# Kernel tuning notes

Hardware: AMD Instinct MI355X
Metric: run time of the kernel (lower is better)

Reference implementation:

```python
import jax, jax.numpy as jnp
import numpy as np

B, S, D, H, HD = 2, 2048, 2048, 16, 128

def _freqs_cis(dim, end, theta=10000.0):
    freqs = 1.0 / theta ** (np.arange(0, dim, 2, dtype=np.float32)[: dim // 2] / dim)
    t = np.arange(end, dtype=np.float32)
    f = np.outer(t, freqs).astype(np.float32)
    f = np.concatenate((f, f), axis=-1)
    return jnp.asarray(np.cos(f)), jnp.asarray(np.sin(f))

def _rotate_half(x):
    x1, x2 = x[..., : x.shape[-1] // 2], x[..., x.shape[-1] // 2 :]
    return jnp.concatenate((-x2, x1), axis=-1)

def setup_inputs() -> dict:
    key = jax.random.key(0)
    ks = jax.random.split(key, 5)
    x = jax.random.normal(ks[0], (B, S, D), jnp.float32)
    scale = 1.0 / np.sqrt(D)
    Wq = jax.random.normal(ks[1], (D, H, HD), jnp.float32) * scale
    Wk = jax.random.normal(ks[2], (D, H, HD), jnp.float32) * scale
    Wv = jax.random.normal(ks[3], (D, H, HD), jnp.float32) * scale
    Wo = jax.random.normal(ks[4], (H, HD, D), jnp.float32) * (1.0 / np.sqrt(D))
    mask = jnp.tril(jnp.ones((S, S), jnp.bool_))[None, None]  # causal [1,1,S,S]
    return {"x": x, "mask": mask, "Wq": Wq, "Wk": Wk, "Wv": Wv, "Wo": Wo}

def reference(x, mask, Wq, Wk, Wv, Wo):
    # QKV projections: [B,S,D] -> [B,S,H,HD]
    q = jnp.einsum('bsd,dhk->bshk', x, Wq)
    k = jnp.einsum('bsd,dhk->bshk', x, Wk)
    v = jnp.einsum('bsd,dhk->bshk', x, Wv)
    # RoPE
    cos, sin = _freqs_cis(HD, x.shape[1])
    cos = cos[None, :, None, :]
    sin = sin[None, :, None, :]
    q = q * cos + _rotate_half(q) * sin
    k = k * cos + _rotate_half(k) * sin
    # scaled dot-product attention
    scores = jnp.einsum('bqhk,bshk->bhqs', q, k) / jnp.sqrt(jnp.asarray(HD, q.dtype))
    big_neg = jnp.finfo(scores.dtype).min
    scores = jnp.where(mask, scores, big_neg)
    attn = jax.nn.softmax(scores, axis=-1)
    ctx = jnp.einsum('bhqs,bshk->bqhk', attn, v)
    # output projection contracting (heads, head_dim)
    return jnp.einsum('bqhk,hkd->bqd', ctx, Wo)
```

## Files before the change

### kernel.cpp

```cpp
#include <hip/hip_runtime.h>

typedef unsigned short u16;
typedef unsigned int u32;

constexpr int Bc = 2, Sc = 2048, Dc = 2048, Hc = 16, HDc = 128;

using short8 = __attribute__((ext_vector_type(8))) short;
using f32x4v = __attribute__((ext_vector_type(4))) float;

static __device__ __forceinline__ float bf2f(u16 v) { return __uint_as_float(((u32)v) << 16); }
static __device__ __forceinline__ u16 f2bf(float f) {
    u32 u = __float_as_uint(f);
    return (u16)((u + 0x7fffu + ((u >> 16) & 1u)) >> 16);
}

__device__ __forceinline__ void gll16(const u16* g, u16* l) {
    __builtin_amdgcn_global_load_lds((const __attribute__((address_space(1))) void*)g,
                                     (__attribute__((address_space(3))) void*)l, 16, 0, 0);
}

__global__ __launch_bounds__(256) void rope_tab_k(float* __restrict__ ctab, float* __restrict__ stab) {
    int idx = blockIdx.x * 256 + threadIdx.x;
    int s = idx >> 6, i = idx & 63;
    float freq = exp2f(-(float)i * 0.20762050593045952f);
    float ang = (float)s * freq;
    float c, sn;
    sincosf(ang, &sn, &c);
    ctab[idx] = c;
    stab[idx] = sn;
}

__global__ __launch_bounds__(256) void cvt_k(const float* __restrict__ in, u16* __restrict__ out, int n) {
    int i = (blockIdx.x * 256 + threadIdx.x) * 8;
    if (i >= n) return;
    float4 a = *(const float4*)(in + i);
    float4 b = *(const float4*)(in + i + 4);
    u16 r[8] = {f2bf(a.x), f2bf(a.y), f2bf(a.z), f2bf(a.w),
                f2bf(b.x), f2bf(b.y), f2bf(b.z), f2bf(b.w)};
    *(uint4*)(out + i) = *(uint4*)r;
}

__global__ __launch_bounds__(256) void tcvt3_k(const float* __restrict__ in0, const float* __restrict__ in1,
                                               const float* __restrict__ in2, u16* __restrict__ out,
                                               int R, int C) {
    __shared__ u16 tile[64][68];
    const float* in = (blockIdx.z == 0) ? in0 : (blockIdx.z == 1) ? in1 : in2;
    u16* o = out + (size_t)blockIdx.z * R * C;
    int bx = blockIdx.x * 64, by = blockIdx.y * 64;
    int t = threadIdx.x;
    int r = t >> 4, c4 = (t & 15) * 4;
    #pragma unroll
    for (int i = 0; i < 4; ++i) {
        int row = by + r + i * 16;
        float4 v = *(const float4*)(in + (size_t)row * C + bx + c4);
        u16* d = &tile[r + i * 16][c4];
        d[0] = f2bf(v.x); d[1] = f2bf(v.y); d[2] = f2bf(v.z); d[3] = f2bf(v.w);
    }
    __syncthreads();
    int oc = t >> 4, r4 = (t & 15) * 4;
    #pragma unroll
    for (int i = 0; i < 4; ++i) {
        int orow = oc + i * 16;
        u16 v[4] = {tile[r4][orow], tile[r4 + 1][orow], tile[r4 + 2][orow], tile[r4 + 3][orow]};
        *(uint2*)&o[(size_t)(bx + orow) * R + by + r4] = *(const uint2*)v;
    }
}

template <int MODE>
__global__ __launch_bounds__(256) void gemm_bt(const u16* __restrict__ A, const u16* __restrict__ Bt,
                                               float* __restrict__ C2, u16* __restrict__ Oq,
                                               u16* __restrict__ Ok, u16* __restrict__ Ov,
                                               const float* __restrict__ ctab,
                                               const float* __restrict__ stab,
                                               int M, int N, int K) {
    __shared__ u16 SM[(MODE == 1) ? 16640 : 8192];
    u16* As = SM;
    u16* Bs = SM + 4096;
    int m0 = blockIdx.y * 128, n0 = blockIdx.x * 128;
    int t = threadIdx.x;
    int wid = t >> 6, lane = t & 63;
    int wr = wid >> 1, wc = wid & 1;
    f32x4v acc[4][4] = {};

    int c0 = wid * 128 + lane;
    int c1 = wid * 128 + 64 + lane;
    const u16* Ar0 = A + (size_t)(m0 + (c0 >> 2)) * K + (((c0 & 3) ^ ((c0 >> 3) & 3)) * 8);
    const u16* Ar1 = A + (size_t)(m0 + (c1 >> 2)) * K + (((c1 & 3) ^ ((c1 >> 3) & 3)) * 8);
    const u16* Br0 = Bt + (size_t)(n0 + (c0 >> 2)) * K + (((c0 & 3) ^ ((c0 >> 3) & 3)) * 8);
    const u16* Br1 = Bt + (size_t)(n0 + (c1 >> 2)) * K + (((c1 & 3) ^ ((c1 >> 3) & 3)) * 8);
    u16* Al0 = As + (size_t)(wid * 128) * 8;
    u16* Al1 = As + (size_t)(wid * 128 + 64) * 8;
    u16* Bl0 = Bs + (size_t)(wid * 128) * 8;
    u16* Bl1 = Bs + (size_t)(wid * 128 + 64) * 8;

    int sw = (lane >> 1) & 3;
    const u16* ap = As + (wr * 64 + (lane & 15)) * 32 + ((((lane >> 4)) ^ sw) << 3);
    const u16* bp = Bs + (wc * 64 + (lane & 15)) * 32 + ((((lane >> 4)) ^ sw) << 3);

    for (int kk = 0; kk < K; kk += 32) {
        gll16(Ar0 + kk, Al0);
        gll16(Ar1 + kk, Al1);
        gll16(Br0 + kk, Bl0);
        gll16(Br1 + kk, Bl1);
        __syncthreads();
        short8 a[4], b[4];
        #pragma unroll
        for (int i = 0; i < 4; ++i) {
            a[i] = *(const short8*)(ap + i * 512);
            b[i] = *(const short8*)(bp + i * 512);
        }
        #pragma unroll
        for (int mf = 0; mf < 4; ++mf)
            #pragma unroll
            for (int nf = 0; nf < 4; ++nf)
                acc[mf][nf] = __builtin_amdgcn_mfma_f32_16x16x32_bf16(a[mf], b[nf], acc[mf][nf], 0, 0, 0);
        __syncthreads();
    }

    int ln = lane & 15, lq = lane >> 4;
    if (MODE == 2) {
        int rb = m0 + wr * 64 + (lq << 2);
        int cb = n0 + wc * 64 + ln;
        #pragma unroll
        for (int mf = 0; mf < 4; ++mf)
            #pragma unroll
            for (int nf = 0; nf < 4; ++nf)
                #pragma unroll
                for (int r = 0; r < 4; ++r)
                    C2[(size_t)(rb + mf * 16 + r) * N + cb + nf * 16] = acc[mf][nf][r];
        return;
    }

    u16* Es = SM;
    {
        int rl0 = wr * 64 + (lq << 2), cl0 = wc * 64 + ln;
        #pragma unroll
        for (int mf = 0; mf < 4; ++mf)
            #pragma unroll
            for (int nf = 0; nf < 4; ++nf)
                #pragma unroll
                for (int r = 0; r < 4; ++r)
                    Es[(rl0 + mf * 16 + r) * 130 + cl0 + nf * 16] = f2bf(acc[mf][nf][r]);
    }
    __syncthreads();

    int which = n0 >> 11;
    int h = (n0 & 2047) >> 7;
    int b_ = m0 >> 11;
    int s0 = m0 & (Sc - 1);

    if (which < 2) {
        u16* dst0 = which ? Ok : Oq;
        int r = t >> 1, h2 = t & 1;
        int s = s0 + r;
        const u16* row = Es + r * 130;
        const float* ct = ctab + (size_t)s * 64;
        const float* st = stab + (size_t)s * 64;
        u16* dp = dst0 + (((size_t)(b_ * Hc + h)) * Sc + s) * HDc + h2 * 64;
        #pragma unroll
        for (int j8 = 0; j8 < 64; j8 += 8) {
            uint4 aa = *(const uint4*)(row + j8);
            uint4 bb = *(const uint4*)(row + 64 + j8);
            const u16* ap8 = (const u16*)&aa;
            const u16* bp8 = (const u16*)&bb;
            float4 c0 = *(const float4*)(ct + j8);
            float4 c1 = *(const float4*)(ct + j8 + 4);
            float4 sn0 = *(const float4*)(st + j8);
            float4 sn1 = *(const float4*)(st + j8 + 4);
            const float* cf = (const float*)&c0;
            float cc[8] = {c0.x, c0.y, c0.z, c0.w, c1.x, c1.y, c1.z, c1.w};
            float ss[8] = {sn0.x, sn0.y, sn0.z, sn0.w, sn1.x, sn1.y, sn1.z, sn1.w};
            (void)cf;
            u16 ov[8];
            #pragma unroll
            for (int e = 0; e < 8; ++e) {
                float x1 = bf2f(ap8[e]), x2 = bf2f(bp8[e]);
                ov[e] = h2 ? f2bf(x2 * cc[e] + x1 * ss[e]) : f2bf(x1 * cc[e] - x2 * ss[e]);
            }
            *(uint4*)(dp + j8) = *(const uint4*)ov;
        }
    } else {
        int d = t >> 1, sh = t & 1;
        u16* dp = Ov + (((size_t)(b_ * Hc + h)) * HDc + d) * Sc + s0 + sh * 64;
        #pragma unroll
        for (int r8 = 0; r8 < 64; r8 += 8) {
            u16 ov[8];
            #pragma unroll
            for (int e = 0; e < 8; ++e)
                ov[e] = Es[(sh * 64 + r8 + e) * 130 + d];
            *(uint4*)(dp + r8) = *(const uint4*)ov;
        }
    }
}

__global__ __launch_bounds__(256) void fattn_k(const u16* __restrict__ Q, const u16* __restrict__ K,
                                               const u16* __restrict__ Vt, u16* __restrict__ ctx) {
    __shared__ u16 KsA[8192];
    __shared__ u16 VsA[8192];
    __shared__ u16 PsA[4 * 32 * 72];
    int t = threadIdx.x, wid = t >> 6, lane = t & 63;
    int bh = blockIdx.x;
    int yt = blockIdx.y;
    int qi = (yt < 8) ? yt : 23 - yt;
    int q0 = qi << 7;
    int wrow0 = q0 + wid * 32;
    const u16* Qb = Q + ((size_t)bh * Sc + wrow0) * HDc;
    const u16* Kb = K + (size_t)bh * Sc * HDc;
    const u16* Vb = Vt + (size_t)bh * HDc * Sc;
    int ln = lane & 15, lq = lane >> 4;
    u16* psw = PsA + wid * 32 * 72;

    short8 aq[2][4];
    #pragma unroll
    for (int mf = 0; mf < 2; ++mf)
        #pragma unroll
        for (int ks = 0; ks < 4; ++ks)
            aq[mf][ks] = *(const short8*)(Qb + (size_t)(mf * 16 + ln) * HDc + ks * 32 + lq * 8);

    short8 onesb;
    {
        short v = (ln == 0) ? (short)0x3F80 : (short)0;
        #pragma unroll
        for (int e = 0; e < 8; ++e) onesb[e] = v;
    }

    f32x4v o[2][8] = {};
    f32x4v lacc[2] = {};

    const float sc = 0.08838834764831845f;
    const float SHIFT = 12.0f;
    int jendw = wrow0 + 31;
    int jendb = q0 + 127;
    int swz = (ln >> 1) & 3;

    for (int j0 = 0; j0 <= jendb; j0 += 64) {
        #pragma unroll
        for (int i = 0; i < 4; ++i) {
            int p = (wid * 4 + i) * 64 + lane;
            int plane = p >> 8, key = (p >> 2) & 63;
            int qc = (p & 3) ^ ((key >> 1) & 3);
            gll16(Kb + (size_t)(j0 + key) * HDc + plane * 32 + qc * 8,
                  KsA + (size_t)(wid * 4 + i) * 512);
        }
        #pragma unroll
        for (int i = 0; i < 4; ++i) {
            int p = (wid * 4 + i) * 64 + lane;
            int plane = p >> 9, d = (p >> 2) & 127;
            int qc = (p & 3) ^ ((d >> 1) & 3);
            gll16(Vb + (size_t)d * Sc + j0 + plane * 32 + qc * 8,
                  VsA + (size_t)(wid * 4 + i) * 512);
        }
        __syncthreads();

        if (j0 <= jendw) {
            f32x4v sf[2][4] = {};
            #pragma unroll
            for (int ks = 0; ks < 4; ++ks)
                #pragma unroll
                for (int nf = 0; nf < 4; ++nf) {
                    short8 bk = *(const short8*)(KsA + ks * 2048 + (nf * 16 + ln) * 32 + ((lq ^ swz) << 3));
                    sf[0][nf] = __builtin_amdgcn_mfma_f32_16x16x32_bf16(aq[0][ks], bk, sf[0][nf], 0, 0, 0);
                    sf[1][nf] = __builtin_amdgcn_mfma_f32_16x16x32_bf16(aq[1][ks], bk, sf[1][nf], 0, 0, 0);
                }

            bool diag = (j0 + 63 > wrow0);
            #pragma unroll
            for (int mf = 0; mf < 2; ++mf) {
                int rowb = mf * 16 + (lq << 2);
                #pragma unroll
                for (int nf = 0; nf < 4; ++nf) {
                    int col = nf * 16 + ln;
                    int ck = col >> 3, cl = col & 7;
                    #pragma unroll
                    for (int r = 0; r < 4; ++r) {
                        float p = __expf(fmaf(sf[mf][nf][r], sc, -SHIFT));
                        if (diag && (j0 + col > wrow0 + rowb + r)) p = 0.f;
                        int row = rowb + r;
                        psw[row * 72 + ((ck ^ (row & 7)) << 3) + cl] = f2bf(p);
                    }
                }
            }

            short8 ap0[2][2];
            #pragma unroll
            for (int mf = 0; mf < 2; ++mf)
                #pragma unroll
                for (int ks = 0; ks < 2; ++ks)
                    ap0[mf][ks] = *(const short8*)(psw + (mf * 16 + ln) * 72 + (((ks * 4 + lq) ^ (ln & 7)) << 3));
            #pragma unroll
            for (int ks = 0; ks < 2; ++ks) {
                lacc[0] = __builtin_amdgcn_mfma_f32_16x16x32_bf16(ap0[0][ks], onesb, lacc[0], 0, 0, 0);
                lacc[1] = __builtin_amdgcn_mfma_f32_16x16x32_bf16(ap0[1][ks], onesb, lacc[1], 0, 0, 0);
                #pragma unroll
                for (int nd = 0; nd < 8; ++nd) {
                    short8 bv = *(const short8*)(VsA + ks * 4096 + (nd * 16 + ln) * 32 + ((lq ^ swz) << 3));
                    o[0][nd] = __builtin_amdgcn_mfma_f32_16x16x32_bf16(ap0[0][ks], bv, o[0][nd], 0, 0, 0);
                    o[1][nd] = __builtin_amdgcn_mfma_f32_16x16x32_bf16(ap0[1][ks], bv, o[1][nd], 0, 0, 0);
                }
            }
        }
        __syncthreads();
    }

    int b = bh >> 4, h = bh & 15;
    #pragma unroll
    for (int mf = 0; mf < 2; ++mf)
        #pragma unroll
        for (int r = 0; r < 4; ++r) {
            float lv = __shfl(lacc[mf][r], lane & 48, 64);
            float inv = 1.0f / lv;
            int q = wrow0 + mf * 16 + (lq << 2) + r;
            u16* cp = ctx + (((size_t)(b * Sc + q)) * Hc + h) * HDc + ln;
            #pragma unroll
            for (int nd = 0; nd < 8; ++nd)
                cp[nd * 16] = f2bf(o[mf][nd][r] * inv);
        }
}

extern "C" void kernel_launch(void* const* d_in, const int* in_sizes, int n_in,
                              void* d_out, int out_size, void* d_ws, size_t ws_size,
                              hipStream_t stream) {
    (void)in_sizes; (void)n_in; (void)out_size; (void)ws_size;
    const float* x  = (const float*)d_in[0];
    const float* Wq = (const float*)d_in[2];
    const float* Wk = (const float*)d_in[3];
    const float* Wv = (const float*)d_in[4];
    const float* Wo = (const float*)d_in[5];

    char* w = (char*)d_ws;
    u16* Wt  = (u16*)w; w += (size_t)3 * Dc * Dc * 2;
    u16* Qb  = (u16*)w; w += (size_t)Bc * Hc * Sc * HDc * 2;
    u16* Kb  = (u16*)w; w += (size_t)Bc * Hc * Sc * HDc * 2;
    u16* Vb  = (u16*)w; w += (size_t)Bc * Hc * Sc * HDc * 2;
    u16* ctx = (u16*)w; w += (size_t)Bc * Sc * Hc * HDc * 2;
    float* ctab = (float*)w; w += (size_t)Sc * 64 * 4;
    float* stab = (float*)w; w += (size_t)Sc * 64 * 4;
    u16* xb = (u16*)d_out;

    rope_tab_k<<<dim3(Sc * 64 / 256), 256, 0, stream>>>(ctab, stab);

    int nx = Bc * Sc * Dc;
    cvt_k<<<dim3(nx / 2048), 256, 0, stream>>>(x, xb, nx);

    tcvt3_k<<<dim3(Dc / 64, Dc / 64, 3), 256, 0, stream>>>(Wq, Wk, Wv, Wt, Dc, Dc);
    gemm_bt<1><<<dim3(3 * Dc / 128, (Bc * Sc) / 128), 256, 0, stream>>>(
        xb, Wt, nullptr, Qb, Kb, Vb, ctab, stab, Bc * Sc, 3 * Dc, Dc);

    fattn_k<<<dim3(Bc * Hc, Sc / 128), 256, 0, stream>>>(Qb, Kb, Vb, ctx);

    tcvt3_k<<<dim3(Dc / 64, Dc / 64, 1), 256, 0, stream>>>(Wo, Wo, Wo, Wt, Dc, Dc);
    gemm_bt<2><<<dim3(Dc / 128, (Bc * Sc) / 128), 256, 0, stream>>>(
        ctx, Wt, (float*)d_out, nullptr, nullptr, nullptr, nullptr, nullptr, Bc * Sc, Dc, Dc);
}
```

Measured before the change: 440.5 us.

## Add 256x256 tiled QKV GEMM with pipelined LDS staging and fused RoPE

Replaces the 128x128 QKV projection GEMM with a new 512-thread kernel that computes 256x256 output tiles. It double-buffers K-slices in LDS through direct global-to-LDS loads, uses an XOR swizzle, and interleaves MFMA quarters with barriers and setprio so memory and compute overlap. The epilogue still applies RoPE and the V transpose, now in two halves through shared memory. The aim is more data reuse per block and better latency hiding, at the cost of higher register and LDS use, fewer blocks in the grid, and hand-tuned waitcnt counts that are fragile.

```diff
diff --git a/kernel.cpp b/kernel.cpp
--- a/kernel.cpp
+++ b/kernel.cpp
@@ -163,14 +163,12 @@
             uint4 bb = *(const uint4*)(row + 64 + j8);
             const u16* ap8 = (const u16*)&aa;
             const u16* bp8 = (const u16*)&bb;
-            float4 c0 = *(const float4*)(ct + j8);
-            float4 c1 = *(const float4*)(ct + j8 + 4);
+            float4 c0f = *(const float4*)(ct + j8);
+            float4 c1f = *(const float4*)(ct + j8 + 4);
             float4 sn0 = *(const float4*)(st + j8);
             float4 sn1 = *(const float4*)(st + j8 + 4);
-            const float* cf = (const float*)&c0;
-            float cc[8] = {c0.x, c0.y, c0.z, c0.w, c1.x, c1.y, c1.z, c1.w};
+            float cc[8] = {c0f.x, c0f.y, c0f.z, c0f.w, c1f.x, c1f.y, c1f.z, c1f.w};
             float ss[8] = {sn0.x, sn0.y, sn0.z, sn0.w, sn1.x, sn1.y, sn1.z, sn1.w};
-            (void)cf;
             u16 ov[8];
             #pragma unroll
             for (int e = 0; e < 8; ++e) {
@@ -190,6 +188,179 @@
                 ov[e] = Es[(sh * 64 + r8 + e) * 130 + d];
             *(uint4*)(dp + r8) = *(const uint4*)ov;
         }
+    }
+}
+
+
+#define FENCE asm volatile("" ::: "memory")
+
+#define RDA(P, mh) do { _Pragma("unroll") for (int m_ = 0; m_ < 4; ++m_) { \
+    aF[m_][0] = *(const short8*)((P) + (mh) * 4096 + m_ * 1024 + co0); \
+    aF[m_][1] = *(const short8*)((P) + (mh) * 4096 + m_ * 1024 + co1); } } while (0)
+
+#define RDB(P, nh) do { _Pragma("unroll") for (int n_ = 0; n_ < 2; ++n_) { \
+    bF[(nh) * 2 + n_][0] = *(const short8*)((P) + ((nh) * 2 + n_) * 1024 + co0); \
+    bF[(nh) * 2 + n_][1] = *(const short8*)((P) + ((nh) * 2 + n_) * 1024 + co1); } } while (0)
+
+#define MFQ(mh, nh) do { _Pragma("unroll") for (int m_ = 0; m_ < 4; ++m_) { \
+    _Pragma("unroll") for (int n_ = 0; n_ < 2; ++n_) { \
+    f32x4v& c_ = acc[(mh) * 4 + m_][(nh) * 2 + n_]; \
+    c_ = __builtin_amdgcn_mfma_f32_16x16x32_bf16(aF[m_][0], bF[(nh) * 2 + n_][0], c_, 0, 0, 0); \
+    c_ = __builtin_amdgcn_mfma_f32_16x16x32_bf16(aF[m_][1], bF[(nh) * 2 + n_][1], c_, 0, 0, 0); } } } while (0)
+
+#define PTAIL(mh, nh) do { FENCE; __builtin_amdgcn_s_barrier(); FENCE; \
+    asm volatile("s_waitcnt lgkmcnt(0)" ::: "memory"); \
+    __builtin_amdgcn_s_setprio(1); MFQ(mh, nh); __builtin_amdgcn_s_setprio(0); \
+    FENCE; __builtin_amdgcn_s_barrier(); FENCE; } while (0)
+
+__global__ __launch_bounds__(512, 2) void gemm256_qkv(
+        const u16* __restrict__ A, const u16* __restrict__ Bt,
+        u16* __restrict__ Oq, u16* __restrict__ Ok, u16* __restrict__ Ov,
+        const float* __restrict__ ctab, const float* __restrict__ stab) {
+    __shared__ u16 SM[65536];
+    constexpr int K = Dc;
+    int t = threadIdx.x, wid = t >> 6, lane = t & 63;
+    int wm = wid >> 2, wn = wid & 3;
+    int ln = lane & 15, lq = lane >> 4;
+
+    int nx = gridDim.x;
+    int lin = blockIdx.y * nx + blockIdx.x;
+    int cpx = (nx * gridDim.y) >> 3;
+    int swzb = (lin & 7) * cpx + (lin >> 3);
+    int n0 = (swzb % nx) << 8;
+    int m0 = (swzb / nx) << 8;
+
+    u16* As0 = SM;
+    u16* As1 = SM + 16384;
+    u16* Bs0 = SM + 32768;
+    u16* Bs1 = SM + 49152;
+
+    auto stage = [&](const u16* G, int r0, int kt, u16* tile, int H) {
+        #pragma unroll
+        for (int L = 0; L < 2; ++L) {
+            int ch16 = H * 1024 + L * 512 + wid * 64 + lane;
+            int row = ch16 >> 3, ch = ch16 & 7;
+            const u16* g = G + (size_t)(r0 + row) * K + kt * 64 + ((ch ^ (row & 7)) << 3);
+            gll16(g, tile + (H * 1024 + L * 512 + wid * 64) * 8);
+        }
+    };
+
+    stage(Bt, n0, 0, Bs0, 0);
+    stage(Bt, n0, 0, Bs0, 1);
+    stage(A,  m0, 0, As0, 0);
+    stage(A,  m0, 0, As0, 1);
+    stage(Bt, n0, 1, Bs1, 0);
+    stage(A,  m0, 1, As1, 0);
+
+    const u16* aR0 = SM + (wm * 128 + ln) * 64;
+    const u16* aR1 = aR0 + 16384;
+    const u16* bR0 = SM + 32768 + (wn * 64 + ln) * 64;
+    const u16* bR1 = bR0 + 16384;
+    int sw = ln & 7;
+    int co0 = (lq ^ sw) << 3;
+    int co1 = ((4 | lq) ^ sw) << 3;
+
+    short8 aF[4][2], bF[4][2];
+    f32x4v acc[8][4] = {};
+
+    asm volatile("s_waitcnt vmcnt(4)" ::: "memory");
+    FENCE; __builtin_amdgcn_s_barrier(); FENCE;
+
+    for (int it = 0; it < K / 128; ++it) {
+        int k1 = (2 * it + 1) & 31, k2 = (2 * it + 2) & 31, k3 = (2 * it + 3) & 31;
+        RDA(aR0, 0); RDB(bR0, 0);
+        stage(Bt, n0, k1, Bs1, 1);
+        asm volatile("s_waitcnt lgkmcnt(8)" ::: "memory");
+        PTAIL(0, 0);
+        RDB(bR0, 1);
+        stage(A, m0, k1, As1, 1);
+        PTAIL(0, 1);
+        RDA(aR0, 1);
+        stage(Bt, n0, k2, Bs0, 0);
+        PTAIL(1, 0);
+        stage(A, m0, k2, As0, 0);
+        asm volatile("s_waitcnt vmcnt(4)" ::: "memory");
+        PTAIL(1, 1);
+        RDA(aR1, 0); RDB(bR1, 0);
+        stage(Bt, n0, k2, Bs0, 1);
+        asm volatile("s_waitcnt lgkmcnt(8)" ::: "memory");
+        PTAIL(0, 0);
+        RDB(bR1, 1);
+        stage(A, m0, k2, As0, 1);
+        PTAIL(0, 1);
+        RDA(aR1, 1);
+        stage(Bt, n0, k3, Bs1, 0);
+        PTAIL(1, 0);
+        stage(A, m0, k3, As1, 0);
+        asm volatile("s_waitcnt vmcnt(4)" ::: "memory");
+        PTAIL(1, 1);
+    }
+    asm volatile("s_waitcnt vmcnt(0)" ::: "memory");
+    __syncthreads();
+
+    int which = n0 >> 11;
+    int h0 = (n0 & 2047) >> 7;
+    int b_ = m0 >> 11;
+    int s0 = m0 & (Sc - 1);
+    u16* Es = SM;
+    const int ESTR = 258;
+
+    #pragma unroll
+    for (int Hh = 0; Hh < 2; ++Hh) {
+        if (wm == Hh) {
+            #pragma unroll
+            for (int mf = 0; mf < 8; ++mf)
+                #pragma unroll
+                for (int nf = 0; nf < 4; ++nf)
+                    #pragma unroll
+                    for (int r = 0; r < 4; ++r)
+                        Es[(mf * 16 + (lq << 2) + r) * ESTR + wn * 64 + nf * 16 + ln] =
+                            f2bf(acc[mf][nf][r]);
+        }
+        __syncthreads();
+        if (which < 2) {
+            u16* dst0 = which ? Ok : Oq;
+            int u = t >> 1, h2 = t & 1;
+            int r = u & 127, hh = u >> 7;
+            int s = s0 + Hh * 128 + r;
+            const u16* rowp = Es + r * ESTR + hh * 128;
+            const float* ct = ctab + (size_t)s * 64;
+            const float* st = stab + (size_t)s * 64;
+            u16* dp = dst0 + (((size_t)(b_ * Hc + h0 + hh)) * Sc + s) * HDc + h2 * 64;
+            #pragma unroll
+            for (int j8 = 0; j8 < 64; j8 += 8) {
+                uint4 aa = *(const uint4*)(rowp + j8);
+                uint4 bb = *(const uint4*)(rowp + 64 + j8);
+                const u16* ap8 = (const u16*)&aa;
+                const u16* bp8 = (const u16*)&bb;
+                float4 c0f = *(const float4*)(ct + j8);
+                float4 c1f = *(const float4*)(ct + j8 + 4);
+                float4 sn0 = *(const float4*)(st + j8);
+                float4 sn1 = *(const float4*)(st + j8 + 4);
+                float cc[8] = {c0f.x, c0f.y, c0f.z, c0f.w, c1f.x, c1f.y, c1f.z, c1f.w};
+                float ss[8] = {sn0.x, sn0.y, sn0.z, sn0.w, sn1.x, sn1.y, sn1.z, sn1.w};
+                u16 ov[8];
+                #pragma unroll
+                for (int e = 0; e < 8; ++e) {
+                    float x1 = bf2f(ap8[e]), x2 = bf2f(bp8[e]);
+                    ov[e] = h2 ? f2bf(x2 * cc[e] + x1 * ss[e]) : f2bf(x1 * cc[e] - x2 * ss[e]);
+                }
+                *(uint4*)(dp + j8) = *(const uint4*)ov;
+            }
+        } else {
+            int u = t >> 1, sh = t & 1;
+            int d = u & 127, hh = u >> 7;
+            u16* dp = Ov + (((size_t)(b_ * Hc + h0 + hh)) * HDc + d) * Sc + s0 + Hh * 128 + sh * 64;
+            #pragma unroll
+            for (int r8 = 0; r8 < 64; r8 += 8) {
+                u16 ov[8];
+                #pragma unroll
+                for (int e = 0; e < 8; ++e)
+                    ov[e] = Es[(sh * 64 + r8 + e) * ESTR + hh * 128 + d];
+                *(uint4*)(dp + r8) = *(const uint4*)ov;
+            }
+        }
+        __syncthreads();
     }
 }
 
@@ -343,8 +514,8 @@
     cvt_k<<<dim3(nx / 2048), 256, 0, stream>>>(x, xb, nx);
 
     tcvt3_k<<<dim3(Dc / 64, Dc / 64, 3), 256, 0, stream>>>(Wq, Wk, Wv, Wt, Dc, Dc);
-    gemm_bt<1><<<dim3(3 * Dc / 128, (Bc * Sc) / 128), 256, 0, stream>>>(
-        xb, Wt, nullptr, Qb, Kb, Vb, ctab, stab, Bc * Sc, 3 * Dc, Dc);
+    gemm256_qkv<<<dim3(3 * Dc / 256, (Bc * Sc) / 256), 512, 0, stream>>>(
+        xb, Wt, Qb, Kb, Vb, ctab, stab);
 
     fattn_k<<<dim3(Bc * Hc, Sc / 128), 256, 0, stream>>>(Qb, Kb, Vb, ctx);
 
```

Result: faster. 424.3 us (-3.7%).

## Replace QKV GEMM with triple-buffered 128x256 tile kernel and XCD-aware block swizzle

Applied to the files above, without the earlier changes.

Adds a dedicated QKV projection GEMM using 512 threads per block and 128x256 output tiles. It stages K in 64-wide slices through a three-stage LDS ring with explicit vmcnt waits, barriers and MFMA priority hints, so loads overlap compute. It also remaps block indices across 8 groups for cache locality. The RoPE/transpose epilogue now handles two heads per block. The cost is much larger LDS use (~144KB) and lower occupancy, which hurts if latency hiding falls short.

```diff
diff --git a/kernel.cpp b/kernel.cpp
--- a/kernel.cpp
+++ b/kernel.cpp
@@ -68,12 +68,9 @@
 
 template <int MODE>
 __global__ __launch_bounds__(256) void gemm_bt(const u16* __restrict__ A, const u16* __restrict__ Bt,
-                                               float* __restrict__ C2, u16* __restrict__ Oq,
-                                               u16* __restrict__ Ok, u16* __restrict__ Ov,
-                                               const float* __restrict__ ctab,
-                                               const float* __restrict__ stab,
+                                               float* __restrict__ C2,
                                                int M, int N, int K) {
-    __shared__ u16 SM[(MODE == 1) ? 16640 : 8192];
+    __shared__ u16 SM[8192];
     u16* As = SM;
     u16* Bs = SM + 4096;
     int m0 = blockIdx.y * 128, n0 = blockIdx.x * 128;
@@ -118,59 +115,160 @@
     }
 
     int ln = lane & 15, lq = lane >> 4;
-    if (MODE == 2) {
-        int rb = m0 + wr * 64 + (lq << 2);
-        int cb = n0 + wc * 64 + ln;
-        #pragma unroll
-        for (int mf = 0; mf < 4; ++mf)
-            #pragma unroll
-            for (int nf = 0; nf < 4; ++nf)
-                #pragma unroll
-                for (int r = 0; r < 4; ++r)
-                    C2[(size_t)(rb + mf * 16 + r) * N + cb + nf * 16] = acc[mf][nf][r];
-        return;
-    }
-
-    u16* Es = SM;
-    {
-        int rl0 = wr * 64 + (lq << 2), cl0 = wc * 64 + ln;
-        #pragma unroll
-        for (int mf = 0; mf < 4; ++mf)
-            #pragma unroll
-            for (int nf = 0; nf < 4; ++nf)
-                #pragma unroll
-                for (int r = 0; r < 4; ++r)
-                    Es[(rl0 + mf * 16 + r) * 130 + cl0 + nf * 16] = f2bf(acc[mf][nf][r]);
-    }
+    int rb = m0 + wr * 64 + (lq << 2);
+    int cb = n0 + wc * 64 + ln;
+    #pragma unroll
+    for (int mf = 0; mf < 4; ++mf)
+        #pragma unroll
+        for (int nf = 0; nf < 4; ++nf)
+            #pragma unroll
+            for (int r = 0; r < 4; ++r)
+                C2[(size_t)(rb + mf * 16 + r) * N + cb + nf * 16] = acc[mf][nf][r];
+}
+
+
+#define FENCE asm volatile("" ::: "memory")
+
+#define RDA8(P) do { _Pragma("unroll") for (int m_ = 0; m_ < 4; ++m_) { \
+    aF[m_][0] = *(const short8*)((P) + m_ * 1024 + co0); \
+    aF[m_][1] = *(const short8*)((P) + m_ * 1024 + co1); } } while (0)
+
+#define RDB2(P, nh) do { _Pragma("unroll") for (int j_ = 0; j_ < 2; ++j_) { \
+    bF[j_][0] = *(const short8*)((P) + ((nh) * 2 + j_) * 1024 + co0); \
+    bF[j_][1] = *(const short8*)((P) + ((nh) * 2 + j_) * 1024 + co1); } } while (0)
+
+#define MFQ8(nh) do { _Pragma("unroll") for (int m_ = 0; m_ < 4; ++m_) \
+    _Pragma("unroll") for (int j_ = 0; j_ < 2; ++j_) { \
+    f32x4v& c_ = acc[m_][(nh) * 2 + j_]; \
+    c_ = __builtin_amdgcn_mfma_f32_16x16x32_bf16(aF[m_][0], bF[j_][0], c_, 0, 0, 0); \
+    c_ = __builtin_amdgcn_mfma_f32_16x16x32_bf16(aF[m_][1], bF[j_][1], c_, 0, 0, 0); } } while (0)
+
+#define PT(nh) do { FENCE; __builtin_amdgcn_s_barrier(); FENCE; \
+    asm volatile("s_waitcnt lgkmcnt(0)" ::: "memory"); \
+    __builtin_amdgcn_s_setprio(1); MFQ8(nh); __builtin_amdgcn_s_setprio(0); \
+    FENCE; __builtin_amdgcn_s_barrier(); FENCE; } while (0)
+
+#define KTILE(aRb, bRb, KST, ADST, BDST, VW) do { \
+    RDA8(aRb); RDB2(bRb, 0); \
+    if ((KST) >= 0) stageA(KST, ADST); \
+    PT(0); \
+    RDB2(bRb, 1); \
+    if ((KST) >= 0) stageB(KST, BDST); \
+    if ((VW) == 6) asm volatile("s_waitcnt vmcnt(6)" ::: "memory"); \
+    else if ((VW) == 0) asm volatile("s_waitcnt vmcnt(0)" ::: "memory"); \
+    PT(1); } while (0)
+
+__global__ __launch_bounds__(512, 2) void gemm128_qkv(
+        const u16* __restrict__ A, const u16* __restrict__ Bt,
+        u16* __restrict__ Oq, u16* __restrict__ Ok, u16* __restrict__ Ov,
+        const float* __restrict__ ctab, const float* __restrict__ stab) {
+    __shared__ u16 SM[73728];
+    constexpr int K = Dc;
+    constexpr int NT = 32;
+    int t = threadIdx.x, wid = t >> 6, lane = t & 63;
+    int wm = wid >> 2, wn = wid & 3;
+    int ln = lane & 15, lq = lane >> 4;
+
+    int nx = gridDim.x;
+    int lin = blockIdx.y * nx + blockIdx.x;
+    int cpx = (nx * gridDim.y) >> 3;
+    int swzb = (lin & 7) * cpx + (lin >> 3);
+    int n0 = (swzb % nx) << 8;
+    int m0 = (swzb / nx) << 7;
+
+    u16* As0 = SM;
+    u16* As1 = SM + 8192;
+    u16* As2 = SM + 16384;
+    u16* Bs0 = SM + 24576;
+    u16* Bs1 = SM + 40960;
+    u16* Bs2 = SM + 57344;
+
+    auto stageA = [&](int kt, u16* dst) {
+        #pragma unroll
+        for (int L = 0; L < 2; ++L) {
+            int ch16 = L * 512 + wid * 64 + lane;
+            int row = ch16 >> 3, ch = ch16 & 7;
+            gll16(A + (size_t)(m0 + row) * K + kt * 64 + ((ch ^ (row & 7)) << 3),
+                  dst + (L * 512 + wid * 64) * 8);
+        }
+    };
+    auto stageB = [&](int kt, u16* dst) {
+        #pragma unroll
+        for (int L = 0; L < 4; ++L) {
+            int ch16 = L * 512 + wid * 64 + lane;
+            int row = ch16 >> 3, ch = ch16 & 7;
+            gll16(Bt + (size_t)(n0 + row) * K + kt * 64 + ((ch ^ (row & 7)) << 3),
+                  dst + (L * 512 + wid * 64) * 8);
+        }
+    };
+
+    const u16* aR0 = As0 + (wm * 64 + ln) * 64;
+    const u16* aR1 = As1 + (wm * 64 + ln) * 64;
+    const u16* aR2 = As2 + (wm * 64 + ln) * 64;
+    const u16* bR0 = Bs0 + (wn * 64 + ln) * 64;
+    const u16* bR1 = Bs1 + (wn * 64 + ln) * 64;
+    const u16* bR2 = Bs2 + (wn * 64 + ln) * 64;
+    int sw = ln & 7;
+    int co0 = (lq ^ sw) << 3;
+    int co1 = ((4 | lq) ^ sw) << 3;
+
+    short8 aF[4][2], bF[2][2];
+    f32x4v acc[4][4] = {};
+
+    stageA(0, As0); stageB(0, Bs0);
+    stageA(1, As1); stageB(1, Bs1);
+    asm volatile("s_waitcnt vmcnt(6)" ::: "memory");
+    FENCE; __builtin_amdgcn_s_barrier(); FENCE;
+
+    for (int k3 = 0; k3 < NT - 2; k3 += 3) {
+        KTILE(aR0, bR0, k3 + 2, As2, Bs2, 6);
+        KTILE(aR1, bR1, k3 + 3, As0, Bs0, 6);
+        KTILE(aR2, bR2, k3 + 4, As1, Bs1, 6);
+    }
+    KTILE(aR0, bR0, -1, As0, Bs0, 0);
+    KTILE(aR1, bR1, -1, As0, Bs0, -1);
+
+    asm volatile("s_waitcnt vmcnt(0)" ::: "memory");
     __syncthreads();
 
     int which = n0 >> 11;
-    int h = (n0 & 2047) >> 7;
+    int h0 = (n0 & 2047) >> 7;
     int b_ = m0 >> 11;
     int s0 = m0 & (Sc - 1);
+    u16* Es = SM;
+    const int ESTR = 258;
+
+    #pragma unroll
+    for (int mf = 0; mf < 4; ++mf)
+        #pragma unroll
+        for (int nf = 0; nf < 4; ++nf)
+            #pragma unroll
+            for (int r = 0; r < 4; ++r)
+                Es[(wm * 64 + mf * 16 + (lq << 2) + r) * ESTR + wn * 64 + nf * 16 + ln] =
+                    f2bf(acc[mf][nf][r]);
+    __syncthreads();
 
     if (which < 2) {
         u16* dst0 = which ? Ok : Oq;
-        int r = t >> 1, h2 = t & 1;
+        int u = t >> 1, h2 = t & 1;
+        int r = u & 127, hh = u >> 7;
         int s = s0 + r;
-        const u16* row = Es + r * 130;
+        const u16* rowp = Es + r * ESTR + hh * 128;
         const float* ct = ctab + (size_t)s * 64;
         const float* st = stab + (size_t)s * 64;
-        u16* dp = dst0 + (((size_t)(b_ * Hc + h)) * Sc + s) * HDc + h2 * 64;
+        u16* dp = dst0 + (((size_t)(b_ * Hc + h0 + hh)) * Sc + s) * HDc + h2 * 64;
         #pragma unroll
         for (int j8 = 0; j8 < 64; j8 += 8) {
-            uint4 aa = *(const uint4*)(row + j8);
-            uint4 bb = *(const uint4*)(row + 64 + j8);
+            uint4 aa = *(const uint4*)(rowp + j8);
+            uint4 bb = *(const uint4*)(rowp + 64 + j8);
             const u16* ap8 = (const u16*)&aa;
             const u16* bp8 = (const u16*)&bb;
-            float4 c0 = *(const float4*)(ct + j8);
-            float4 c1 = *(const float4*)(ct + j8 + 4);
+            float4 c0f = *(const float4*)(ct + j8);
+            float4 c1f = *(const float4*)(ct + j8 + 4);
             float4 sn0 = *(const float4*)(st + j8);
             float4 sn1 = *(const float4*)(st + j8 + 4);
-            const float* cf = (const float*)&c0;
-            float cc[8] = {c0.x, c0.y, c0.z, c0.w, c1.x, c1.y, c1.z, c1.w};
+            float cc[8] = {c0f.x, c0f.y, c0f.z, c0f.w, c1f.x, c1f.y, c1f.z, c1f.w};
             float ss[8] = {sn0.x, sn0.y, sn0.z, sn0.w, sn1.x, sn1.y, sn1.z, sn1.w};
-            (void)cf;
             u16 ov[8];
             #pragma unroll
             for (int e = 0; e < 8; ++e) {
@@ -180,14 +278,15 @@
             *(uint4*)(dp + j8) = *(const uint4*)ov;
         }
     } else {
-        int d = t >> 1, sh = t & 1;
-        u16* dp = Ov + (((size_t)(b_ * Hc + h)) * HDc + d) * Sc + s0 + sh * 64;
+        int u = t >> 1, sh = t & 1;
+        int d = u & 127, hh = u >> 7;
+        u16* dp = Ov + (((size_t)(b_ * Hc + h0 + hh)) * HDc + d) * Sc + s0 + sh * 64;
         #pragma unroll
         for (int r8 = 0; r8 < 64; r8 += 8) {
             u16 ov[8];
             #pragma unroll
             for (int e = 0; e < 8; ++e)
-                ov[e] = Es[(sh * 64 + r8 + e) * 130 + d];
+                ov[e] = Es[(sh * 64 + r8 + e) * ESTR + hh * 128 + d];
             *(uint4*)(dp + r8) = *(const uint4*)ov;
         }
     }
@@ -343,12 +442,12 @@
     cvt_k<<<dim3(nx / 2048), 256, 0, stream>>>(x, xb, nx);
 
     tcvt3_k<<<dim3(Dc / 64, Dc / 64, 3), 256, 0, stream>>>(Wq, Wk, Wv, Wt, Dc, Dc);
-    gemm_bt<1><<<dim3(3 * Dc / 128, (Bc * Sc) / 128), 256, 0, stream>>>(
-        xb, Wt, nullptr, Qb, Kb, Vb, ctab, stab, Bc * Sc, 3 * Dc, Dc);
+    gemm128_qkv<<<dim3(3 * Dc / 256, (Bc * Sc) / 128), 512, 0, stream>>>(
+        xb, Wt, Qb, Kb, Vb, ctab, stab);
 
     fattn_k<<<dim3(Bc * Hc, Sc / 128), 256, 0, stream>>>(Qb, Kb, Vb, ctx);
 
     tcvt3_k<<<dim3(Dc / 64, Dc / 64, 1), 256, 0, stream>>>(Wo, Wo, Wo, Wt, Dc, Dc);
     gemm_bt<2><<<dim3(Dc / 128, (Bc * Sc) / 128), 256, 0, stream>>>(
-        ctx, Wt, (float*)d_out, nullptr, nullptr, nullptr, nullptr, nullptr, Bc * Sc, Dc, Dc);
-}
+        ctx, Wt, (float*)d_out, Bc * Sc, Dc, Dc);
+}
```

After: 424.2 us. 3.7% less time.
